# Kernel optimization log

Hardware: AMD Instinct MI355X
Metric: run time of the kernel (lower is better)

The kernel has to match this reference:

```python
import jax, jax.numpy as jnp
import numpy as np

EPS = 1e-6
NUM_HEADS = 12


def _layernorm(x, eps=EPS):
    m = jnp.mean(x, axis=-1, keepdims=True)
    v = jnp.var(x, axis=-1, keepdims=True)
    return (x - m) * jax.lax.rsqrt(v + eps)


def _rmsnorm(x, w, eps=EPS):
    ms = jnp.mean(jnp.square(x), axis=-1, keepdims=True)
    return x * jax.lax.rsqrt(ms + eps) * w


def _rope_interleaved(x, cos, sin):
    # x: [B, L, H, hd]; cos/sin: [L, hd//2]; is_neox_style=False (interleaved pairs)
    x1 = x[..., 0::2]
    x2 = x[..., 1::2]
    c = cos[None, :, None, :]
    s = sin[None, :, None, :]
    o1 = x1 * c - x2 * s
    o2 = x1 * s + x2 * c
    return jnp.stack([o1, o2], axis=-1).reshape(x.shape)


def _attention(q, k, v, mask=None):
    # q: [B, Lq, H, hd], k/v: [B, Lk, H, hd]
    hd = q.shape[-1]
    scale = 1.0 / jnp.sqrt(jnp.asarray(hd, q.dtype))
    scores = jnp.einsum('blhd,bmhd->bhlm', q, k) * scale
    if mask is not None:
        scores = jnp.where(mask[None, None], scores, jnp.finfo(scores.dtype).min)
    p = jax.nn.softmax(scores, axis=-1)
    return jnp.einsum('bhlm,bmhd->blhd', p, v)


def setup_inputs() -> dict:
    key = jax.random.key(0)
    B, F, FS, D, FF, LC = 1, 2, 1560, 1536, 8960, 512
    L = F * FS
    hd = D // NUM_HEADS
    ks = jax.random.split(key, 32)
    i = iter(range(32))
    n = lambda shape, s=0.02: jax.random.normal(ks[next(i)], shape, jnp.float32) * s
    inp = {
        'hidden_states': n((B, L, D), 1.0),
        'encoder_hidden_states': n((B, LC, D), 1.0),
        'temb': n((B, F, 6, D), 1.0),
    }
    pos = jnp.arange(L, dtype=jnp.float32)
    inv = 1.0 / (10000.0 ** (jnp.arange(hd // 2, dtype=jnp.float32) / (hd // 2)))
    ang = pos[:, None] * inv[None, :]
    inp['cos'] = jnp.cos(ang)
    inp['sin'] = jnp.sin(ang)
    fidx = jnp.arange(L) // FS
    inp['attn_mask'] = fidx[:, None] >= fidx[None, :]  # frame-level block-causal
    # params
    inp['sst'] = n((1, 6, D), 1.0 / np.sqrt(D))
    for name in ['wq', 'wk', 'wv', 'wo']:
        inp[name] = n((D, D))
    for name in ['bq', 'bk', 'bv', 'bo']:
        inp[name] = jnp.zeros((D,), jnp.float32)
    inp['nq_w'] = jnp.ones((D,), jnp.float32)
    inp['nk_w'] = jnp.ones((D,), jnp.float32)
    inp['ln2_g'] = jnp.ones((D,), jnp.float32)
    inp['ln2_b'] = jnp.zeros((D,), jnp.float32)
    for name in ['cwq', 'cwk', 'cwv', 'cwo']:
        inp[name] = n((D, D))
    for name in ['cbq', 'cbk', 'cbv', 'cbo']:
        inp[name] = jnp.zeros((D,), jnp.float32)
    inp['cnq_w'] = jnp.ones((D,), jnp.float32)
    inp['cnk_w'] = jnp.ones((D,), jnp.float32)
    inp['w1'] = n((D, FF))
    inp['b1'] = jnp.zeros((FF,), jnp.float32)
    inp['w2'] = n((FF, D))
    inp['b2'] = jnp.zeros((D,), jnp.float32)
    return inp


def reference(hidden_states, encoder_hidden_states, temb, cos, sin, attn_mask,
              sst, wq, bq, wk, bk, wv, bv, wo, bo, nq_w, nk_w, ln2_g, ln2_b,
              cwq, cbq, cwk, cbk, cwv, cbv, cwo, cbo, cnq_w, cnk_w,
              w1, b1, w2, b2):
    B, L, D = hidden_states.shape
    F = temb.shape[1]
    FS = L // F
    H = NUM_HEADS
    hd = D // H

    e = sst[:, None] + temb  # [B, F, 6, D]
    shift_msa, scale_msa, gate_msa = e[:, :, 0], e[:, :, 1], e[:, :, 2]
    c_shift, c_scale, c_gate = e[:, :, 3], e[:, :, 4], e[:, :, 5]

    # --- self attention ---
    nh = _layernorm(hidden_states).reshape(B, F, FS, D)
    nh = (nh * (1.0 + scale_msa[:, :, None]) + shift_msa[:, :, None]).reshape(B, L, D)
    q = _rmsnorm(nh @ wq + bq, nq_w).reshape(B, L, H, hd)
    k = _rmsnorm(nh @ wk + bk, nk_w).reshape(B, L, H, hd)
    v = (nh @ wv + bv).reshape(B, L, H, hd)
    q = _rope_interleaved(q, cos, sin)
    k = _rope_interleaved(k, cos, sin)
    attn_out = _attention(q, k, v, attn_mask).reshape(B, L, D) @ wo + bo

    h = hidden_states + (attn_out.reshape(B, F, FS, D) * gate_msa[:, :, None]).reshape(B, L, D)
    norm_h = _layernorm(h) * ln2_g + ln2_b  # null shift/scale

    # --- cross attention ---
    LC = encoder_hidden_states.shape[1]
    cq = _rmsnorm(norm_h @ cwq + cbq, cnq_w).reshape(B, L, H, hd)
    ck = _rmsnorm(encoder_hidden_states @ cwk + cbk, cnk_w).reshape(B, LC, H, hd)
    cv = (encoder_hidden_states @ cwv + cbv).reshape(B, LC, H, hd)
    cross_out = _attention(cq, ck, cv).reshape(B, L, D) @ cwo + cbo

    h = h + cross_out  # gate = 1
    norm_h = _layernorm(h).reshape(B, F, FS, D)
    norm_h = (norm_h * (1.0 + c_scale[:, :, None]) + c_shift[:, :, None]).reshape(B, L, D)

    # --- ffn ---
    ff = jax.nn.gelu(norm_h @ w1 + b1, approximate=True) @ w2 + b2
    h = h + (ff.reshape(B, F, FS, D) * c_gate[:, :, None]).reshape(B, L, D)
    return h
```

## Files before the change

### kernel.cpp

```cpp
#include <hip/hip_runtime.h>
#include <hip/hip_bf16.h>
#include <math.h>

typedef __bf16 bf16;
typedef __bf16 bf16x8 __attribute__((ext_vector_type(8)));
typedef float  f32x4  __attribute__((ext_vector_type(4)));
typedef unsigned int u32;

#define DMODEL 1536
#define NHEADS 12
#define HD 128
#define HDH 64

__device__ __forceinline__ void async16(const void* g, void* l) {
  __builtin_amdgcn_global_load_lds((const __attribute__((address_space(1))) u32*)g,
                                   (__attribute__((address_space(3))) u32*)l, 16, 0, 0);
}

__device__ inline void block_reduce2(float& a, float& b) {
  __shared__ float sa[4], sb[4];
  #pragma unroll
  for (int off = 32; off; off >>= 1) {
    a += __shfl_xor(a, off);
    b += __shfl_xor(b, off);
  }
  int w = threadIdx.x >> 6;
  if ((threadIdx.x & 63) == 0) { sa[w] = a; sb[w] = b; }
  __syncthreads();
  a = sa[0] + sa[1] + sa[2] + sa[3];
  b = sb[0] + sb[1] + sb[2] + sb[3];
  __syncthreads();
}

__global__ __launch_bounds__(256)
void ln_kernel(const float* __restrict__ X, bf16* __restrict__ Y,
               const float* __restrict__ sst, const float* __restrict__ temb,
               const float* __restrict__ g, const float* __restrict__ bvec,
               int jshift, int jscale, int FS, int mode)
{
  int row = blockIdx.x;
  const float* x = X + (size_t)row * DMODEL;
  float v[6];
  float s1 = 0.f, s2 = 0.f;
  #pragma unroll
  for (int i = 0; i < 6; i++) {
    float t = x[threadIdx.x + i * 256];
    v[i] = t; s1 += t; s2 += t * t;
  }
  block_reduce2(s1, s2);
  float mean = s1 * (1.f / DMODEL);
  float var  = s2 * (1.f / DMODEL) - mean * mean;
  float rs = rsqrtf(var + 1e-6f);
  int f = row / FS;
  bf16* y = Y + (size_t)row * DMODEL;
  #pragma unroll
  for (int i = 0; i < 6; i++) {
    int d = threadIdx.x + i * 256;
    float t = (v[i] - mean) * rs;
    float o;
    if (mode == 0) {
      float sc = sst[jscale * DMODEL + d] + temb[(f * 6 + jscale) * DMODEL + d];
      float sh = sst[jshift * DMODEL + d] + temb[(f * 6 + jshift) * DMODEL + d];
      o = t * (1.f + sc) + sh;
    } else {
      o = t * g[d] + bvec[d];
    }
    y[d] = (bf16)o;
  }
}

__global__ __launch_bounds__(256)
void rms_rope_kernel(const float* __restrict__ P, int S, long long MN,
                     const bf16* __restrict__ Xb, int RS, int CO,
                     const float* __restrict__ bias, bf16* __restrict__ Y,
                     const float* __restrict__ w,
                     const float* __restrict__ cosb, const float* __restrict__ sinb,
                     int dorope, float oscale)
{
  __shared__ float rowbuf[DMODEL];
  int row = blockIdx.x;
  float v[6];
  float s2 = 0.f, dummy = 0.f;
  if (Xb) {
    const bf16* x = Xb + (size_t)row * RS + CO;
    #pragma unroll
    for (int i = 0; i < 6; i++) {
      int d = threadIdx.x + i * 256;
      float t = (float)x[d];
      v[i] = t; rowbuf[d] = t; s2 += t * t;
    }
  } else {
    const float* x = P + (size_t)row * RS + CO;
    #pragma unroll
    for (int i = 0; i < 6; i++) {
      int d = threadIdx.x + i * 256;
      float t = bias[d];
      for (int s = 0; s < S; s++) t += x[(size_t)s * MN + d];
      v[i] = t; rowbuf[d] = t; s2 += t * t;
    }
  }
  __syncthreads();
  block_reduce2(s2, dummy);
  float rs = rsqrtf(s2 * (1.f / DMODEL) + 1e-6f) * oscale;
  bf16* y = Y + (size_t)row * DMODEL;
  if (dorope) {
    #pragma unroll
    for (int i = 0; i < 3; i++) {
      int p = threadIdx.x + i * 256;
      int d0 = 2 * p, d1 = 2 * p + 1;
      float y0 = rowbuf[d0] * rs * w[d0];
      float y1 = rowbuf[d1] * rs * w[d1];
      int ih = p & 63;
      float c = cosb[(size_t)row * HDH + ih];
      float s = sinb[(size_t)row * HDH + ih];
      y[d0] = (bf16)(y0 * c - y1 * s);
      y[d1] = (bf16)(y0 * s + y1 * c);
    }
  } else {
    #pragma unroll
    for (int i = 0; i < 6; i++) {
      int d = threadIdx.x + i * 256;
      y[d] = (bf16)(v[i] * rs * w[d]);
    }
  }
}

__global__ __launch_bounds__(256)
void wt_kernel(const float* __restrict__ W, bf16* __restrict__ Wt, int K, int N)
{
  __shared__ float T[32][33];
  int k0 = blockIdx.x * 32, n0 = blockIdx.y * 32;
  int tx = threadIdx.x & 31, ty = threadIdx.x >> 5;
  #pragma unroll
  for (int i = 0; i < 4; i++)
    T[ty + 8 * i][tx] = W[(size_t)(k0 + ty + 8 * i) * N + n0 + tx];
  __syncthreads();
  #pragma unroll
  for (int i = 0; i < 4; i++)
    Wt[(size_t)(n0 + ty + 8 * i) * K + k0 + tx] = (bf16)T[tx][ty + 8 * i];
}

__global__ __launch_bounds__(256)
void catbias_kernel(float* __restrict__ bqkv, const float* __restrict__ bq,
                    const float* __restrict__ bk, const float* __restrict__ bv,
                    float* __restrict__ cbkv, const float* __restrict__ cbk,
                    const float* __restrict__ cbv)
{
  int i = blockIdx.x * 256 + threadIdx.x;
  if (i < DMODEL) {
    bqkv[i] = bq[i]; bqkv[DMODEL + i] = bk[i]; bqkv[2 * DMODEL + i] = bv[i];
    cbkv[i] = cbk[i]; cbkv[DMODEL + i] = cbv[i];
  }
}

__global__ __launch_bounds__(256)
void gemm_bt(const bf16* __restrict__ A, const bf16* __restrict__ Bt,
             const float* __restrict__ bias, float* __restrict__ Cf,
             bf16* __restrict__ Cb, int M, int N, int K, int act,
             int Ks, long long MN)
{
  __shared__ bf16 As[128 * 32];
  __shared__ bf16 Bs[128 * 32];
  int tid = threadIdx.x, lane = tid & 63, w = tid >> 6;
  int wm = w >> 1, wn = w & 1;
  int l16 = lane & 15, quad = lane >> 4;

  int gx = (M + 127) >> 7, gy = N >> 7;
  int per_panel = gx << 3;
  int bid = blockIdx.x;
  int panel = bid / per_panel;
  int rem = bid - panel * per_panel;
  int pc0 = panel << 3;
  int ncols = gy - pc0; if (ncols > 8) ncols = 8;
  int by = pc0 + rem % ncols;
  int bx = rem / ncols;
  int bm = bx * 128, bn = by * 128;

  int kb0 = blockIdx.y * Ks;

  int rl = lane >> 2;
  int kk = (lane & 3) * 8;
  int r0 = (2 * w) * 16 + rl, r1 = (2 * w + 1) * 16 + rl;
  int am0 = bm + r0; if (am0 > M - 1) am0 = M - 1;
  int am1 = bm + r1; if (am1 > M - 1) am1 = M - 1;
  const bf16* a0 = A + (size_t)am0 * K + kk;
  const bf16* a1 = A + (size_t)am1 * K + kk;
  const bf16* b0 = Bt + (size_t)(bn + r0) * K + kk;
  const bf16* b1 = Bt + (size_t)(bn + r1) * K + kk;
  bf16* lA0 = As + (2 * w) * 512; bf16* lA1 = As + (2 * w + 1) * 512;
  bf16* lB0 = Bs + (2 * w) * 512; bf16* lB1 = Bs + (2 * w + 1) * 512;

  f32x4 acc[4][4] = {};
  int kend = kb0 + Ks;
  for (int k0 = kb0; k0 < kend; k0 += 32) {
    async16(a0 + k0, lA0);
    async16(a1 + k0, lA1);
    async16(b0 + k0, lB0);
    async16(b1 + k0, lB1);
    __syncthreads();
    bf16x8 af[4], bfv[4];
    #pragma unroll
    for (int mi = 0; mi < 4; mi++)
      af[mi] = *(const bf16x8*)&As[(wm * 64 + mi * 16 + l16) * 32 + quad * 8];
    #pragma unroll
    for (int ni = 0; ni < 4; ni++)
      bfv[ni] = *(const bf16x8*)&Bs[(wn * 64 + ni * 16 + l16) * 32 + quad * 8];
    #pragma unroll
    for (int mi = 0; mi < 4; mi++)
      #pragma unroll
      for (int ni = 0; ni < 4; ni++)
        acc[mi][ni] = __builtin_amdgcn_mfma_f32_16x16x32_bf16(af[mi], bfv[ni], acc[mi][ni], 0, 0, 0);
    __syncthreads();
  }
  float* Cfo = Cf ? Cf + (size_t)blockIdx.y * MN : nullptr;
  #pragma unroll
  for (int mi = 0; mi < 4; mi++) {
    #pragma unroll
    for (int r = 0; r < 4; r++) {
      int m = bm + wm * 64 + mi * 16 + quad * 4 + r;
      if (m < M) {
        #pragma unroll
        for (int ni = 0; ni < 4; ni++) {
          int n = bn + wn * 64 + ni * 16 + l16;
          float val = acc[mi][ni][r] + (bias ? bias[n] : 0.f);
          if (act == 1) {
            float u = val + 0.044715f * val * val * val;
            float z = 1.5957691216057308f * u;
            val = val / (1.f + __expf(-z));
          }
          if (Cfo) Cfo[(size_t)m * N + n] = val;
          else     Cb[(size_t)m * N + n] = (bf16)val;
        }
      }
    }
  }
}

__global__ __launch_bounds__(512, 2)
void gemm256(const bf16* __restrict__ A, const bf16* __restrict__ Bt,
             const float* __restrict__ bias, float* __restrict__ Cf,
             bf16* __restrict__ Cb, int M, int N, int K, int act,
             int S, long long MN)
{
  __shared__ bf16 LDS[2][2][128 * 128];
  int tid = threadIdx.x, lane = tid & 63, w = tid >> 6;
  int wm = w >> 2, wn = w & 3;
  int l16 = lane & 15, quad = lane >> 4;

  int gmx = (M + 255) >> 8, gny = N >> 8;
  int per_panel = gmx << 3;
  int bid = blockIdx.x;
  int panel = bid / per_panel;
  int rem = bid - panel * per_panel;
  int pc0 = panel << 3;
  int ncols = gny - pc0; if (ncols > 8) ncols = 8;
  int by = pc0 + rem % ncols;
  int bx = rem / ncols;
  int bm = bx << 8, bn = by << 8;

  int NTtot = K >> 6;
  int sidx = blockIdx.y;
  int basek = NTtot / S, remk = NTtot % S;
  int NT = basek + (sidx < remk ? 1 : 0);
  int t0k = sidx * basek + (sidx < remk ? sidx : remk);
  int kb0 = t0k << 6;

  int aro = (l16 * 64 + quad * 16) ^ ((l16 >> 3) << 5);
  const char* A0r = (const char*)&LDS[0][0][0] + wm * 16384 + aro;
  const char* A1r = (const char*)&LDS[1][0][0] + wm * 16384 + aro;
  const char* B0r = (const char*)&LDS[0][1][0] + wn * 8192 + aro;
  const char* B1r = (const char*)&LDS[1][1][0] + wn * 8192 + aro;

  int srl = lane >> 2;
  int sc16 = (lane & 3) ^ (((lane >> 5) & 1) << 1);
  int Mm1 = M - 1, Nm1 = N - 1;
  int ga0 = bm + w * 16 + srl;        if (ga0 > Mm1) ga0 = Mm1;
  int ga1 = bm + 128 + w * 16 + srl;  if (ga1 > Mm1) ga1 = Mm1;
  int gb0 = bn + w * 16 + srl;        if (gb0 > Nm1) gb0 = Nm1;
  int gb1 = bn + 128 + w * 16 + srl;  if (gb1 > Nm1) gb1 = Nm1;
  const bf16* Ag0 = A + (size_t)ga0 * K + sc16 * 8;
  const bf16* Ag1 = A + (size_t)ga1 * K + sc16 * 8;
  const bf16* Bg0 = Bt + (size_t)gb0 * K + sc16 * 8;
  const bf16* Bg1 = Bt + (size_t)gb1 * K + sc16 * 8;
  char* wA0[2] = { (char*)&LDS[0][0][0] + w * 2048, (char*)&LDS[1][0][0] + w * 2048 };
  char* wA1[2] = { wA0[0] + 16384, wA0[1] + 16384 };
  char* wB0[2] = { (char*)&LDS[0][1][0] + w * 2048, (char*)&LDS[1][1][0] + w * 2048 };
  char* wB1[2] = { wB0[0] + 16384, wB0[1] + 16384 };

#define STG(src, kk_, dst) do { const bf16* _s = (src) + (kk_); \
    async16(_s, (dst)); async16(_s + 32, (dst) + 1024); } while (0)
#define MFMA_(d, a, b) d = __builtin_amdgcn_mfma_f32_16x16x32_bf16(a, b, d, 0, 0, 0)

  STG(Ag0, kb0, wA0[0]); STG(Ag1, kb0, wA1[0]);
  STG(Bg0, kb0, wB0[0]); STG(Bg1, kb0, wB1[0]);
  asm volatile("s_waitcnt vmcnt(0)" ::: "memory");
  __builtin_amdgcn_s_barrier();

  f32x4 acc[8][4] = {};
  for (int t = 0; t < NT; ++t) {
    int b = t & 1;
    const char* Ab = b ? A1r : A0r;
    const char* Bb = b ? B1r : B0r;
    bool st1 = (t + 1) < NT;
    if (st1) {
      int kt = kb0 + (t + 1) * 64;
      STG(Ag0, kt, wA0[b ^ 1]); STG(Ag1, kt, wA1[b ^ 1]);
      STG(Bg0, kt, wB0[b ^ 1]); STG(Bg1, kt, wB1[b ^ 1]);
    }
    bf16x8 b0v[4], b1v[4], a0[8];
    #pragma unroll
    for (int i = 0; i < 4; i++) b0v[i] = *(const bf16x8*)(Bb + i * 1024);
    #pragma unroll
    for (int i = 0; i < 4; i++) b1v[i] = *(const bf16x8*)(Bb + (4 + i) * 1024);
    #pragma unroll
    for (int i = 0; i < 8; i++) a0[i] = *(const bf16x8*)(Ab + i * 1024);
    #pragma unroll
    for (int mi = 0; mi < 4; mi++) {
      #pragma unroll
      for (int ni = 0; ni < 2; ni++) {
        MFMA_(acc[mi][ni],     a0[mi * 2],     b0v[ni * 2]);
        MFMA_(acc[mi][ni],     a0[mi * 2 + 1], b0v[ni * 2 + 1]);
        MFMA_(acc[mi][2 + ni], a0[mi * 2],     b1v[ni * 2]);
        MFMA_(acc[mi][2 + ni], a0[mi * 2 + 1], b1v[ni * 2 + 1]);
      }
    }
    bf16x8 a1[8];
    #pragma unroll
    for (int i = 0; i < 8; i++) a1[i] = *(const bf16x8*)(Ab + (8 + i) * 1024);
    #pragma unroll
    for (int mi = 0; mi < 4; mi++) {
      #pragma unroll
      for (int ni = 0; ni < 2; ni++) {
        MFMA_(acc[4 + mi][ni],     a1[mi * 2],     b0v[ni * 2]);
        MFMA_(acc[4 + mi][ni],     a1[mi * 2 + 1], b0v[ni * 2 + 1]);
        MFMA_(acc[4 + mi][2 + ni], a1[mi * 2],     b1v[ni * 2]);
        MFMA_(acc[4 + mi][2 + ni], a1[mi * 2 + 1], b1v[ni * 2 + 1]);
      }
    }
    if (st1) { asm volatile("s_waitcnt vmcnt(0)" ::: "memory"); }
    __builtin_amdgcn_s_barrier();
  }
#undef STG
#undef MFMA_

  float* Cfo = Cf ? Cf + (size_t)blockIdx.y * MN : nullptr;
  #pragma unroll
  for (int mi = 0; mi < 8; mi++) {
    #pragma unroll
    for (int r = 0; r < 4; r++) {
      int m = bm + wm * 128 + mi * 16 + quad * 4 + r;
      if (m < M) {
        #pragma unroll
        for (int ni = 0; ni < 4; ni++) {
          int n = bn + wn * 64 + ni * 16 + l16;
          float val = acc[mi][ni][r] + (bias ? bias[n] : 0.f);
          if (act == 1) {
            float u = val + 0.044715f * val * val * val;
            float z = 1.5957691216057308f * u;
            val = val / (1.f + __expf(-z));
          }
          if (Cfo) Cfo[(size_t)m * N + n] = val;
          else     Cb[(size_t)m * N + n] = (bf16)val;
        }
      }
    }
  }
}

__global__ __launch_bounds__(256)
void transposev_kernel(const bf16* __restrict__ Xb, int RS, int CO,
                       bf16* __restrict__ Vt, int L)
{
  __shared__ bf16 T[64][65];
  int l0 = blockIdx.x * 64, n0 = blockIdx.y * 64;
  int tid = threadIdx.x;
  int r = tid >> 2;
  int c8 = (tid & 3) * 16;
  int lc = l0 + r; if (lc > L - 1) lc = L - 1;
  const bf16* src = Xb + (size_t)lc * RS + CO + n0 + c8;
  #pragma unroll
  for (int i = 0; i < 16; i++) T[r][c8 + i] = src[i];
  __syncthreads();
  #pragma unroll
  for (int i = 0; i < 16; i++) {
    int l = l0 + c8 + i;
    if (l < L) Vt[(size_t)(n0 + r) * L + l] = T[c8 + i][r];
  }
}

__global__ __launch_bounds__(256)
void flash2_kernel(const bf16* __restrict__ Q, const bf16* __restrict__ Kg,
                   const bf16* __restrict__ Vt, bf16* __restrict__ O,
                   int Lq, int Lk, int FS, int causal, int nqb)
{
  __shared__ bf16 Kt[64 * 128];
  __shared__ bf16 Vtile[128 * 64];
  __shared__ bf16 Pl[4][16][72];
  int tid = threadIdx.x, lane = tid & 63, w = tid >> 6;
  int l16 = lane & 15, quad = lane >> 4;
  int bid = blockIdx.x;
  int h = bid % NHEADS;
  int qb = nqb - 1 - (bid / NHEADS);
  int q0b = qb * 64;
  int q0w = q0b + w * 16;

  int qrow = q0w + l16; if (qrow > Lq - 1) qrow = Lq - 1;
  const bf16* qbase = Q + (size_t)qrow * DMODEL + h * HD + quad * 8;
  bf16x8 qf[4];
  #pragma unroll
  for (int dc = 0; dc < 4; dc++) qf[dc] = *(const bf16x8*)(qbase + dc * 32);

  int kvrow[4];
  int kvmin_w = Lk, kv_end = Lk;
  if (causal) {
    #pragma unroll
    for (int r = 0; r < 4; r++) {
      int qr = q0w + quad * 4 + r; if (qr > Lq - 1) qr = Lq - 1;
      kvrow[r] = (qr / FS + 1) * FS;
    }
    int q0c = q0w; if (q0c > Lq - 1) q0c = Lq - 1;
    kvmin_w = (q0c / FS + 1) * FS;
    int qlast = q0b + 63; if (qlast > Lq - 1) qlast = Lq - 1;
    kv_end = (qlast / FS + 1) * FS;
    if (kv_end > Lk) kv_end = Lk;
  }

  f32x4 acc_o[8] = {};
  float m_i[4], l_i[4];
  #pragma unroll
  for (int r = 0; r < 4; r++) { m_i[r] = -1e30f; l_i[r] = 0.f; }

  for (int kb = 0; kb < kv_end; kb += 64) {
    #pragma unroll
    for (int j = 0; j < 4; j++) {
      int u = w * 256 + j * 64 + lane;
      int row = u >> 4;
      int c = (u & 15) ^ (row & 15);
      int krow = kb + row; if (krow > Lk - 1) krow = Lk - 1;
      async16(Kg + (size_t)krow * DMODEL + h * HD + c * 8,
              Kt + (size_t)(w * 256 + j * 64) * 8);
    }
    #pragma unroll
    for (int j = 0; j < 4; j++) {
      int u = w * 256 + j * 64 + lane;
      int row = u >> 3;
      int c = (u & 7) ^ (row & 7);
      async16(Vt + (size_t)(h * HD + row) * Lk + kb + c * 8,
              Vtile + (size_t)(w * 256 + j * 64) * 8);
    }
    __syncthreads();

    f32x4 s[4] = {};
    #pragma unroll
    for (int nk = 0; nk < 4; nk++) {
      #pragma unroll
      for (int dc = 0; dc < 4; dc++) {
        bf16x8 kf = *(const bf16x8*)&Kt[(((nk * 16 + l16) << 4) + ((4 * dc + quad) ^ l16)) * 8];
        s[nk] = __builtin_amdgcn_mfma_f32_16x16x32_bf16(qf[dc], kf, s[nk], 0, 0, 0);
      }
    }

    bool need_mask = causal && (kb + 64 > kvmin_w);
    float p[4][4];
    #pragma unroll
    for (int r = 0; r < 4; r++) {
      #pragma unroll
      for (int nk = 0; nk < 4; nk++) {
        float sv = s[nk][r];
        if (need_mask && (kb + nk * 16 + l16 >= kvrow[r])) sv = -1e30f;
        p[nk][r] = sv;
      }
      float bm = fmaxf(fmaxf(p[0][r], p[1][r]), fmaxf(p[2][r], p[3][r]));
      #pragma unroll
      for (int off = 8; off; off >>= 1) bm = fmaxf(bm, __shfl_xor(bm, off));
      float mn = fmaxf(m_i[r], bm);
      float alpha = __expf(m_i[r] - mn);
      m_i[r] = mn;
      float ps = 0.f;
      #pragma unroll
      for (int nk = 0; nk < 4; nk++) {
        float e = __expf(p[nk][r] - mn);
        p[nk][r] = e; ps += e;
      }
      #pragma unroll
      for (int off = 8; off; off >>= 1) ps += __shfl_xor(ps, off);
      l_i[r] = l_i[r] * alpha + ps;
      #pragma unroll
      for (int t = 0; t < 8; t++) acc_o[t][r] *= alpha;
    }

    #pragma unroll
    for (int nk = 0; nk < 4; nk++)
      #pragma unroll
      for (int r = 0; r < 4; r++)
        Pl[w][quad * 4 + r][nk * 16 + l16] = (bf16)p[nk][r];
    __threadfence_block();
    bf16x8 pf0 = *(const bf16x8*)&Pl[w][l16][quad * 8];
    bf16x8 pf1 = *(const bf16x8*)&Pl[w][l16][32 + quad * 8];

    #pragma unroll
    for (int t = 0; t < 8; t++) {
      bf16x8 vf0 = *(const bf16x8*)&Vtile[(((t * 16 + l16) << 3) + ((quad) ^ (l16 & 7))) * 8];
      bf16x8 vf1 = *(const bf16x8*)&Vtile[(((t * 16 + l16) << 3) + ((4 + quad) ^ (l16 & 7))) * 8];
      acc_o[t] = __builtin_amdgcn_mfma_f32_16x16x32_bf16(pf0, vf0, acc_o[t], 0, 0, 0);
      acc_o[t] = __builtin_amdgcn_mfma_f32_16x16x32_bf16(pf1, vf1, acc_o[t], 0, 0, 0);
    }
    __syncthreads();
  }

  #pragma unroll
  for (int r = 0; r < 4; r++) {
    int m = q0w + quad * 4 + r;
    if (m < Lq) {
      float inv = 1.f / l_i[r];
      bf16* obase = O + (size_t)m * DMODEL + h * HD;
      #pragma unroll
      for (int t = 0; t < 8; t++)
        obase[t * 16 + l16] = (bf16)(acc_o[t][r] * inv);
    }
  }
}

__global__ __launch_bounds__(256)
void modresid_kernel(const float* __restrict__ base, const float* __restrict__ P,
                     int S, long long MN, const float* __restrict__ bias,
                     float* __restrict__ out,
                     const float* __restrict__ sst, const float* __restrict__ temb,
                     int jg, int FS, long long total)
{
  long long i = (long long)blockIdx.x * 256 + threadIdx.x;
  if (i >= total) return;
  int d = (int)(i % DMODEL);
  int f = (int)((i / DMODEL) / FS);
  float g = sst[jg * DMODEL + d] + temb[(f * 6 + jg) * DMODEL + d];
  float v = bias[d];
  for (int s = 0; s < S; s++) v += P[(size_t)s * MN + i];
  out[i] = base[i] + v * g;
}

__global__ __launch_bounds__(256)
void addf_kernel(float* __restrict__ h, const float* __restrict__ P,
                 int S, long long MN, const float* __restrict__ bias, long long total)
{
  long long i = (long long)blockIdx.x * 256 + threadIdx.x;
  if (i >= total) return;
  int d = (int)(i % DMODEL);
  float v = bias[d];
  for (int s = 0; s < S; s++) v += P[(size_t)s * MN + i];
  h[i] += v;
}

__global__ __launch_bounds__(256)
void cast_kernel(const float* __restrict__ x, bf16* __restrict__ y, long long total)
{
  long long i = (long long)blockIdx.x * 256 + threadIdx.x;
  if (i < total) y[i] = (bf16)x[i];
}

extern "C" void kernel_launch(void* const* d_in, const int* in_sizes, int n_in,
                              void* d_out, int out_size, void* d_ws, size_t ws_size,
                              hipStream_t stream)
{
  const float* hs   = (const float*)d_in[0];
  const float* enc  = (const float*)d_in[1];
  const float* temb = (const float*)d_in[2];
  const float* cosb = (const float*)d_in[3];
  const float* sinb = (const float*)d_in[4];
  const float* sst  = (const float*)d_in[6];
  const float* wq = (const float*)d_in[7];
  const float* wk = (const float*)d_in[8];
  const float* wv = (const float*)d_in[9];
  const float* wo = (const float*)d_in[10];
  const float* bq = (const float*)d_in[11];
  const float* bk = (const float*)d_in[12];
  const float* bv = (const float*)d_in[13];
  const float* bo = (const float*)d_in[14];
  const float* nq_w = (const float*)d_in[15];
  const float* nk_w = (const float*)d_in[16];
  const float* ln2_g = (const float*)d_in[17];
  const float* ln2_b = (const float*)d_in[18];
  const float* cwq = (const float*)d_in[19];
  const float* cwk = (const float*)d_in[20];
  const float* cwv = (const float*)d_in[21];
  const float* cwo = (const float*)d_in[22];
  const float* cbq = (const float*)d_in[23];
  const float* cbk = (const float*)d_in[24];
  const float* cbv = (const float*)d_in[25];
  const float* cbo = (const float*)d_in[26];
  const float* cnq_w = (const float*)d_in[27];
  const float* cnk_w = (const float*)d_in[28];
  const float* w1 = (const float*)d_in[29];
  const float* b1 = (const float*)d_in[30];
  const float* w2 = (const float*)d_in[31];
  const float* b2 = (const float*)d_in[32];

  int L  = in_sizes[0] / DMODEL;
  int LC = in_sizes[1] / DMODEL;
  int F  = in_sizes[2] / (6 * DMODEL);
  int FS = L / F;
  int FF = in_sizes[30];
  long long LD = (long long)L * DMODEL;
  float* outp = (float*)d_out;
  int N3 = 3 * DMODEL, N2 = 2 * DMODEL;

  char* p = (char*)d_ws;
  auto alloc = [&](size_t bytes) -> char* {
    char* r = p; p += (bytes + 255) & ~(size_t)255; return r;
  };
  size_t DD = (size_t)DMODEL * DMODEL;
  bf16* wqkv_t = (bf16*)alloc(DD * 3 * 2);
  bf16* wto_t  = (bf16*)alloc(DD * 2);
  bf16* cwq_t  = (bf16*)alloc(DD * 2);
  bf16* cwkv_t = (bf16*)alloc(DD * 2 * 2);
  bf16* cwo_t  = (bf16*)alloc(DD * 2);
  bf16* w1t = (bf16*)alloc((size_t)DMODEL * FF * 2);
  bf16* w2t = (bf16*)alloc((size_t)DMODEL * FF * 2);
  float* bqkv = (float*)alloc((size_t)N3 * 4);
  float* cbkv = (float*)alloc((size_t)N2 * 4);
  float* hbuf = (float*)alloc((size_t)LD * 4);
  bf16* nh   = (bf16*)alloc((size_t)LD * 2);
  bf16* qb   = (bf16*)alloc((size_t)LD * 2);
  bf16* kb   = (bf16*)alloc((size_t)LD * 2);
  bf16* ab   = (bf16*)alloc((size_t)LD * 2);
  bf16* vtc  = (bf16*)alloc((size_t)LC * DMODEL * 2);
  bf16* encb = (bf16*)alloc((size_t)LC * DMODEL * 2);
  char* BIG1 = alloc((size_t)L * FF * 2);
  bf16* qkvb = (bf16*)BIG1;
  bf16* ckvb = (bf16*)BIG1;
  bf16* ffb  = (bf16*)BIG1;
  char* BIG2 = alloc((size_t)LD * 3 * 4);
  bf16* vtb = (bf16*)BIG2;
  float* Pp = (float*)BIG2;
  (void)ws_size; (void)n_in; (void)out_size;

  dim3 gWdd(DMODEL / 32, DMODEL / 32);
  wt_kernel<<<gWdd, 256, 0, stream>>>(wq, wqkv_t, DMODEL, DMODEL);
  wt_kernel<<<gWdd, 256, 0, stream>>>(wk, wqkv_t + DD, DMODEL, DMODEL);
  wt_kernel<<<gWdd, 256, 0, stream>>>(wv, wqkv_t + 2 * DD, DMODEL, DMODEL);
  wt_kernel<<<gWdd, 256, 0, stream>>>(wo, wto_t, DMODEL, DMODEL);
  wt_kernel<<<gWdd, 256, 0, stream>>>(cwq, cwq_t, DMODEL, DMODEL);
  wt_kernel<<<gWdd, 256, 0, stream>>>(cwk, cwkv_t, DMODEL, DMODEL);
  wt_kernel<<<gWdd, 256, 0, stream>>>(cwv, cwkv_t + DD, DMODEL, DMODEL);
  wt_kernel<<<gWdd, 256, 0, stream>>>(cwo, cwo_t, DMODEL, DMODEL);
  wt_kernel<<<dim3(DMODEL / 32, FF / 32), 256, 0, stream>>>(w1, w1t, DMODEL, FF);
  wt_kernel<<<dim3(FF / 32, DMODEL / 32), 256, 0, stream>>>(w2, w2t, FF, DMODEL);
  catbias_kernel<<<6, 256, 0, stream>>>(bqkv, bq, bk, bv, cbkv, cbk, cbv);

  int gxC = (LC + 127) / 128;
  int gmx = (L + 255) / 256;
  int ewg = (int)((LD + 255) / 256);
  int nqb = (L + 63) / 64;
  const float qs = 0.08838834764831845f;

  ln_kernel<<<L, 256, 0, stream>>>(hs, nh, sst, temb, nullptr, nullptr, 0, 1, FS, 0);
  gemm256<<<dim3(gmx * (N3 / 256), 1), 512, 0, stream>>>(nh, wqkv_t, bqkv, nullptr, qkvb,
                                                         L, N3, DMODEL, 0, 1, 0);
  rms_rope_kernel<<<L, 256, 0, stream>>>(nullptr, 0, 0, qkvb, N3, 0, nullptr, qb, nq_w, cosb, sinb, 1, qs);
  rms_rope_kernel<<<L, 256, 0, stream>>>(nullptr, 0, 0, qkvb, N3, DMODEL, nullptr, kb, nk_w, cosb, sinb, 1, 1.0f);
  transposev_kernel<<<dim3((L + 63) / 64, DMODEL / 64), 256, 0, stream>>>(qkvb, N3, 2 * DMODEL, vtb, L);
  flash2_kernel<<<NHEADS * nqb, 256, 0, stream>>>(qb, kb, vtb, ab, L, L, FS, 1, nqb);
  gemm256<<<dim3(gmx * (DMODEL / 256), 3), 512, 0, stream>>>(ab, wto_t, nullptr, Pp, nullptr,
                                                             L, DMODEL, DMODEL, 0, 3, LD);
  modresid_kernel<<<ewg, 256, 0, stream>>>(hs, Pp, 3, LD, bo, hbuf, sst, temb, 2, FS, LD);
  ln_kernel<<<L, 256, 0, stream>>>(hbuf, nh, nullptr, nullptr, ln2_g, ln2_b, 0, 0, FS, 1);
  gemm256<<<dim3(gmx * (DMODEL / 256), 3), 512, 0, stream>>>(nh, cwq_t, nullptr, Pp, nullptr,
                                                             L, DMODEL, DMODEL, 0, 3, LD);
  rms_rope_kernel<<<L, 256, 0, stream>>>(Pp, 3, LD, nullptr, DMODEL, 0, cbq, qb, cnq_w, nullptr, nullptr, 0, qs);
  cast_kernel<<<(int)(((long long)LC * DMODEL + 255) / 256), 256, 0, stream>>>(enc, encb, (long long)LC * DMODEL);
  gemm_bt<<<dim3(gxC * (N2 / 128), 1), 256, 0, stream>>>(encb, cwkv_t, cbkv, nullptr, ckvb,
                                                         LC, N2, DMODEL, 0, DMODEL, 0);
  rms_rope_kernel<<<LC, 256, 0, stream>>>(nullptr, 0, 0, ckvb, N2, 0, nullptr, kb, cnk_w, nullptr, nullptr, 0, 1.0f);
  transposev_kernel<<<dim3((LC + 63) / 64, DMODEL / 64), 256, 0, stream>>>(ckvb, N2, DMODEL, vtc, LC);
  flash2_kernel<<<NHEADS * nqb, 256, 0, stream>>>(qb, kb, vtc, ab, L, LC, FS, 0, nqb);
  gemm256<<<dim3(gmx * (DMODEL / 256), 3), 512, 0, stream>>>(ab, cwo_t, nullptr, Pp, nullptr,
                                                             L, DMODEL, DMODEL, 0, 3, LD);
  addf_kernel<<<ewg, 256, 0, stream>>>(hbuf, Pp, 3, LD, cbo, LD);
  ln_kernel<<<L, 256, 0, stream>>>(hbuf, nh, sst, temb, nullptr, nullptr, 3, 4, FS, 0);
  gemm256<<<dim3(gmx * (FF / 256), 1), 512, 0, stream>>>(nh, w1t, b1, nullptr, ffb,
                                                         L, FF, DMODEL, 1, 1, 0);
  gemm256<<<dim3(gmx * (DMODEL / 256), 3), 512, 0, stream>>>(ffb, w2t, nullptr, Pp, nullptr,
                                                             L, DMODEL, FF, 0, 3, LD);
  modresid_kernel<<<ewg, 256, 0, stream>>>(hbuf, Pp, 3, LD, b2, outp, sst, temb, 5, FS, LD);
}
```

Measured before the change: 1.095 ms.

## Deepen gemm256 pipeline to four-stage LDS ring with BK=32 tiles

The 256x256 GEMM now uses a four-slot LDS ring of K=32 tiles in place of double-buffered K=64 tiles. It keeps up to three tiles of global_load_lds in flight and waits with partial vmcnt counts, so loads overlap more MFMA work. The cost is twice as many barriers per unit of K and fewer MFMAs between syncs. It also changes the LDS addressing and swizzle usage, which could affect bank conflicts.

```diff
diff --git a/kernel.cpp b/kernel.cpp
--- a/kernel.cpp
+++ b/kernel.cpp
@@ -242,7 +242,7 @@
              bf16* __restrict__ Cb, int M, int N, int K, int act,
              int S, long long MN)
 {
-  __shared__ bf16 LDS[2][2][128 * 128];
+  __shared__ bf16 LDS[4][2][16 * 512];
   int tid = threadIdx.x, lane = tid & 63, w = tid >> 6;
   int wm = w >> 2, wn = w & 3;
   int l16 = lane & 15, quad = lane >> 4;
@@ -258,18 +258,15 @@
   int bx = rem / ncols;
   int bm = bx << 8, bn = by << 8;
 
-  int NTtot = K >> 6;
+  int NTtot = K >> 5;
   int sidx = blockIdx.y;
   int basek = NTtot / S, remk = NTtot % S;
   int NT = basek + (sidx < remk ? 1 : 0);
   int t0k = sidx * basek + (sidx < remk ? sidx : remk);
-  int kb0 = t0k << 6;
+  int kb0 = t0k << 5;
 
   int aro = (l16 * 64 + quad * 16) ^ ((l16 >> 3) << 5);
-  const char* A0r = (const char*)&LDS[0][0][0] + wm * 16384 + aro;
-  const char* A1r = (const char*)&LDS[1][0][0] + wm * 16384 + aro;
-  const char* B0r = (const char*)&LDS[0][1][0] + wn * 8192 + aro;
-  const char* B1r = (const char*)&LDS[1][1][0] + wn * 8192 + aro;
+  char* ldsb = (char*)&LDS[0][0][0];
 
   int srl = lane >> 2;
   int sc16 = (lane & 3) ^ (((lane >> 5) & 1) << 1);
@@ -278,67 +275,43 @@
   int ga1 = bm + 128 + w * 16 + srl;  if (ga1 > Mm1) ga1 = Mm1;
   int gb0 = bn + w * 16 + srl;        if (gb0 > Nm1) gb0 = Nm1;
   int gb1 = bn + 128 + w * 16 + srl;  if (gb1 > Nm1) gb1 = Nm1;
-  const bf16* Ag0 = A + (size_t)ga0 * K + sc16 * 8;
-  const bf16* Ag1 = A + (size_t)ga1 * K + sc16 * 8;
-  const bf16* Bg0 = Bt + (size_t)gb0 * K + sc16 * 8;
-  const bf16* Bg1 = Bt + (size_t)gb1 * K + sc16 * 8;
-  char* wA0[2] = { (char*)&LDS[0][0][0] + w * 2048, (char*)&LDS[1][0][0] + w * 2048 };
-  char* wA1[2] = { wA0[0] + 16384, wA0[1] + 16384 };
-  char* wB0[2] = { (char*)&LDS[0][1][0] + w * 2048, (char*)&LDS[1][1][0] + w * 2048 };
-  char* wB1[2] = { wB0[0] + 16384, wB0[1] + 16384 };
-
-#define STG(src, kk_, dst) do { const bf16* _s = (src) + (kk_); \
-    async16(_s, (dst)); async16(_s + 32, (dst) + 1024); } while (0)
+  const bf16* Ag0 = A + (size_t)ga0 * K + kb0 + sc16 * 8;
+  const bf16* Ag1 = A + (size_t)ga1 * K + kb0 + sc16 * 8;
+  const bf16* Bg0 = Bt + (size_t)gb0 * K + kb0 + sc16 * 8;
+  const bf16* Bg1 = Bt + (size_t)gb1 * K + kb0 + sc16 * 8;
+
+#define STG(tt) do { int _k = (tt) * 32; char* _d = ldsb + ((tt) & 3) * 32768 + w * 1024; \
+    async16(Ag0 + _k, _d);          async16(Ag1 + _k, _d + 8192); \
+    async16(Bg0 + _k, _d + 16384);  async16(Bg1 + _k, _d + 24576); } while (0)
 #define MFMA_(d, a, b) d = __builtin_amdgcn_mfma_f32_16x16x32_bf16(a, b, d, 0, 0, 0)
 
-  STG(Ag0, kb0, wA0[0]); STG(Ag1, kb0, wA1[0]);
-  STG(Bg0, kb0, wB0[0]); STG(Bg1, kb0, wB1[0]);
-  asm volatile("s_waitcnt vmcnt(0)" ::: "memory");
+  STG(0);
+  if (NT > 1) STG(1);
+  if (NT > 2) STG(2);
+  if (NT > 2)      { asm volatile("s_waitcnt vmcnt(8)" ::: "memory"); }
+  else if (NT > 1) { asm volatile("s_waitcnt vmcnt(4)" ::: "memory"); }
+  else             { asm volatile("s_waitcnt vmcnt(0)" ::: "memory"); }
   __builtin_amdgcn_s_barrier();
 
   f32x4 acc[8][4] = {};
   for (int t = 0; t < NT; ++t) {
-    int b = t & 1;
-    const char* Ab = b ? A1r : A0r;
-    const char* Bb = b ? B1r : B0r;
-    bool st1 = (t + 1) < NT;
-    if (st1) {
-      int kt = kb0 + (t + 1) * 64;
-      STG(Ag0, kt, wA0[b ^ 1]); STG(Ag1, kt, wA1[b ^ 1]);
-      STG(Bg0, kt, wB0[b ^ 1]); STG(Bg1, kt, wB1[b ^ 1]);
-    }
-    bf16x8 b0v[4], b1v[4], a0[8];
-    #pragma unroll
-    for (int i = 0; i < 4; i++) b0v[i] = *(const bf16x8*)(Bb + i * 1024);
-    #pragma unroll
-    for (int i = 0; i < 4; i++) b1v[i] = *(const bf16x8*)(Bb + (4 + i) * 1024);
-    #pragma unroll
-    for (int i = 0; i < 8; i++) a0[i] = *(const bf16x8*)(Ab + i * 1024);
-    #pragma unroll
-    for (int mi = 0; mi < 4; mi++) {
-      #pragma unroll
-      for (int ni = 0; ni < 2; ni++) {
-        MFMA_(acc[mi][ni],     a0[mi * 2],     b0v[ni * 2]);
-        MFMA_(acc[mi][ni],     a0[mi * 2 + 1], b0v[ni * 2 + 1]);
-        MFMA_(acc[mi][2 + ni], a0[mi * 2],     b1v[ni * 2]);
-        MFMA_(acc[mi][2 + ni], a0[mi * 2 + 1], b1v[ni * 2 + 1]);
-      }
-    }
-    bf16x8 a1[8];
-    #pragma unroll
-    for (int i = 0; i < 8; i++) a1[i] = *(const bf16x8*)(Ab + (8 + i) * 1024);
-    #pragma unroll
-    for (int mi = 0; mi < 4; mi++) {
-      #pragma unroll
-      for (int ni = 0; ni < 2; ni++) {
-        MFMA_(acc[4 + mi][ni],     a1[mi * 2],     b0v[ni * 2]);
-        MFMA_(acc[4 + mi][ni],     a1[mi * 2 + 1], b0v[ni * 2 + 1]);
-        MFMA_(acc[4 + mi][2 + ni], a1[mi * 2],     b1v[ni * 2]);
-        MFMA_(acc[4 + mi][2 + ni], a1[mi * 2 + 1], b1v[ni * 2 + 1]);
-      }
-    }
-    if (st1) { asm volatile("s_waitcnt vmcnt(0)" ::: "memory"); }
-    __builtin_amdgcn_s_barrier();
+    if (t + 3 < NT) STG(t + 3);
+    const char* Ar = ldsb + (t & 3) * 32768 + wm * 8192 + aro;
+    const char* Br = ldsb + (t & 3) * 32768 + 16384 + wn * 4096 + aro;
+    bf16x8 a[8], bv[4];
+    #pragma unroll
+    for (int i = 0; i < 4; i++) bv[i] = *(const bf16x8*)(Br + i * 1024);
+    #pragma unroll
+    for (int i = 0; i < 8; i++) a[i] = *(const bf16x8*)(Ar + i * 1024);
+    #pragma unroll
+    for (int mi = 0; mi < 8; mi++)
+      #pragma unroll
+      for (int ni = 0; ni < 4; ni++)
+        MFMA_(acc[mi][ni], a[mi], bv[ni]);
+    int remt = NT - 1 - t;
+    if (remt >= 3)      { asm volatile("s_waitcnt vmcnt(8)" ::: "memory"); __builtin_amdgcn_s_barrier(); }
+    else if (remt == 2) { asm volatile("s_waitcnt vmcnt(4)" ::: "memory"); __builtin_amdgcn_s_barrier(); }
+    else if (remt == 1) { asm volatile("s_waitcnt vmcnt(0)" ::: "memory"); __builtin_amdgcn_s_barrier(); }
   }
 #undef STG
 #undef MFMA_
```

Result: no change. 1.092 ms (-0.2%).
